# Performance work log

Measured on AMD Instinct MI355X. Metric: run time of the kernel, lower is better.

The kernel has to match this reference:

```python
import jax, jax.numpy as jnp
import numpy as np

B, S, D_MODEL = 1, 1024, 1024
D_CKV, D_CQ = 256, 512
N_HEAD, D_HEAD, D_ROPE = 8, 64, 32


def setup_inputs() -> dict:
    key = jax.random.key(0)
    ks = jax.random.split(key, 12)
    def w(k, shape):
        return jax.random.normal(k, shape, dtype=jnp.float32) * 0.02
    return {
        "x": jax.random.normal(ks[0], (B, S, D_MODEL), dtype=jnp.float32),
        "w_q_idx": w(ks[1], (D_MODEL, N_HEAD * D_HEAD)),
        "w_k_idx": w(ks[2], (D_MODEL, D_HEAD)),
        "w_idx": jnp.ones((N_HEAD,), dtype=jnp.float32),
        "raw_delta": jnp.zeros((D_ROPE // 2,), dtype=jnp.float32),
        "w_dkv": w(ks[3], (D_MODEL, D_CKV)),
        "w_uk": w(ks[4], (D_CKV, N_HEAD * D_HEAD)),
        "w_uv": w(ks[5], (D_CKV, N_HEAD * D_HEAD)),
        "w_dq": w(ks[6], (D_MODEL, D_CQ)),
        "w_uq": w(ks[7], (D_CQ, N_HEAD * D_HEAD)),
        "w_qr": w(ks[8], (D_CQ, N_HEAD * D_ROPE)),
        "w_kr": w(ks[9], (D_MODEL, D_ROPE)),
        "w_out": w(ks[10], (N_HEAD * D_HEAD, D_MODEL)),
        "k_ts": 128,
        "local_window": 64,
    }


def _pope(x, raw_delta, theta):
    # x: (b, L, H, d_rope); positions run along axis 1 (matches torch PoPE)
    delta = -2.0 * jnp.pi * jax.nn.sigmoid(raw_delta)            # (d2,)
    pos = jnp.arange(x.shape[1], dtype=x.dtype)
    ang = pos[None, :, None, None] * theta + delta               # (1, L, 1, d2)
    c, s = jnp.cos(ang), jnp.sin(ang)
    mu1, mu2 = jnp.split(jax.nn.softplus(x), 2, axis=-1)
    return jnp.concatenate((mu1 * c - mu2 * s, mu1 * s + mu2 * c), axis=-1)


def reference(x, w_q_idx, w_k_idx, w_idx, raw_delta, w_dkv, w_uk, w_uv,
              w_dq, w_uq, w_qr, w_kr, w_out, k_ts, local_window):
    b, s, _ = x.shape
    h, dh, dr = N_HEAD, D_HEAD, D_ROPE
    theta = 1.0 / (10000.0 ** (2.0 * jnp.arange(dr // 2, dtype=jnp.float32) / dr))

    # ---- LightningIndexer: per-head relu'd relevance, combined with learned head weights
    qI = (x @ w_q_idx).reshape(b, s, h, dh)
    kI = x @ w_k_idx                                             # (b, s, dh)
    sc = jax.nn.relu(jnp.einsum('bthd,bsd->bths', qI, kI))
    I = jnp.einsum('bths,h->bts', sc, w_idx)

    # ---- TokenSelector: force local window in, mask future out, top-k indices
    qp = jnp.arange(s)[:, None]
    kp = jnp.arange(s)[None, :]
    local = (kp >= qp - local_window + 1) & (kp <= qp)
    causal = kp > qp
    I = jnp.where(local, jnp.inf, I)
    I = jnp.where(causal, -jnp.inf, I)
    k = min(k_ts, s)
    _, idx = jax.lax.top_k(I, k)                                 # (b, s, k) int32

    gather = jax.vmap(lambda t, i: t[i])                         # (s,d),(l,k)->(l,k,d)

    # ---- MLA latent KV, gathered per query
    c_kv = x @ w_dkv                                             # (b, s, d_ckv)
    ckv_sel = gather(c_kv, idx)                                  # (b, s, k, d_ckv)
    key_c = (ckv_sel @ w_uk).reshape(b, s, k, h, dh).transpose(0, 3, 1, 2, 4)
    value = (ckv_sel @ w_uv).reshape(b, s, k, h, dh).transpose(0, 3, 1, 2, 4)

    c_q = x @ w_dq
    query_c = (c_q @ w_uq).reshape(b, s, h, dh).transpose(0, 2, 1, 3)
    query_r = _pope((c_q @ w_qr).reshape(b, s, h, dr), raw_delta, theta).transpose(0, 2, 1, 3)

    # key rope: PoPE applied with positions along the k (selected-token) axis,
    # exactly as the torch code's permute(0,2,1,3) does
    x_sel = gather(x, idx)                                       # (b, s, k, d_model)
    kr = _pope((x_sel @ w_kr).transpose(0, 2, 1, 3), raw_delta, theta).transpose(0, 2, 1, 3)
    key_r = jnp.broadcast_to(kr[:, None], (b, h, s, k, dr))

    query = jnp.concatenate((query_c, query_r), axis=-1)         # (b, h, s, dh+dr)
    keyt = jnp.concatenate((key_c, key_r), axis=-1)              # (b, h, s, k, dh+dr)
    scale = (dh + dr) ** -0.5
    scores = jnp.einsum('bhld,bhlkd->bhlk', query, keyt) * scale
    attn = jax.nn.softmax(scores, axis=-1)
    out = jnp.einsum('bhlk,bhlkd->bhld', attn, value)
    out = out.transpose(0, 2, 1, 3).reshape(b, s, h * dh)
    return out @ w_out
```

## Files before the change

kernel.cpp:

```cpp
#include <hip/hip_runtime.h>
#include <math.h>

#define S_LEN 1024
#define NH 8

typedef __attribute__((ext_vector_type(8))) short bf16x8;
typedef __attribute__((ext_vector_type(4))) float f32x4;

__device__ __forceinline__ float sp_softplus(float x) {
    return fmaxf(x, 0.f) + log1pf(expf(-fabsf(x)));
}

__device__ __forceinline__ unsigned short bfu(float f) {
    unsigned u = __float_as_uint(f);
    unsigned r = (u + 0x7FFFu + ((u >> 16) & 1u)) >> 16;
    return (unsigned short)r;
}

struct FRONT {
    const float *x, *wqidx, *wkidx, *raw_delta, *wuk;
    const float *wdkv, *wdq, *wkr, *wuq, *wqr, *wuv, *wout;
    float *qIP, *kIP, *csc, *css;
    unsigned short *wdkvT, *wdqT, *wkrT, *wuqT, *wqrT, *wuvT, *woutT, *wukb;
};

__global__ __launch_bounds__(256) void front_kernel(FRONT f)
{
    __shared__ float As[2][16][18];
    __shared__ float Bs[2][16][68];
    __shared__ unsigned short tile[64][65];
    int bx = blockIdx.x;
    if (bx < 1152) {
        int gx = bx % 18, gy = bx / 18;
        int half = threadIdx.x >> 7;
        int t = threadIdx.x & 127;
        int u = gx * 2 + half;
        const float* B; float* C;
        int ldb, N, n0, kb;
        if (u < 32) {
            B = f.wqidx; ldb = 512; N = 512;
            C = f.qIP + (long)(u >> 3) * 524288;
            n0 = (u & 7) * 64;
            kb = (u >> 3) * 256;
        } else {
            B = f.wkidx; ldb = 64; N = 64;
            C = f.kIP + (long)(u - 32) * 65536;
            n0 = 0;
            kb = (u - 32) * 256;
        }
        int ke = kb + 256;
        int m0 = gy * 16;
        int ar = t >> 2, ak = t & 3;
        int bk = t >> 3, bn = t & 7;
        int ty = t >> 4, tx = t & 15;

        float4 aN = make_float4(0.f, 0.f, 0.f, 0.f);
        if (t < 64) aN = *(const float4*)(f.x + (long)(m0 + ar) * 1024 + kb + ak * 4);
        float4 b0 = *(const float4*)(B + (long)(kb + bk) * ldb + n0 + bn * 4);
        float4 b1 = *(const float4*)(B + (long)(kb + bk) * ldb + n0 + (bn + 8) * 4);
        float acc[2][4] = {};
        for (int k0 = kb; k0 < ke; k0 += 16) {
            if (t < 64) {
                As[half][ak * 4 + 0][ar] = aN.x;
                As[half][ak * 4 + 1][ar] = aN.y;
                As[half][ak * 4 + 2][ar] = aN.z;
                As[half][ak * 4 + 3][ar] = aN.w;
            }
            *(float4*)&Bs[half][bk][bn * 4] = b0;
            *(float4*)&Bs[half][bk][(bn + 8) * 4] = b1;
            __syncthreads();
            if (k0 + 16 < ke) {
                if (t < 64) aN = *(const float4*)(f.x + (long)(m0 + ar) * 1024 + (k0 + 16) + ak * 4);
                b0 = *(const float4*)(B + (long)(k0 + 16 + bk) * ldb + n0 + bn * 4);
                b1 = *(const float4*)(B + (long)(k0 + 16 + bk) * ldb + n0 + (bn + 8) * 4);
            }
            #pragma unroll
            for (int kk = 0; kk < 16; ++kk) {
                float2 a = *(float2*)&As[half][kk][ty * 2];
                float4 b = *(float4*)&Bs[half][kk][tx * 4];
                acc[0][0] += a.x * b.x; acc[0][1] += a.x * b.y;
                acc[0][2] += a.x * b.z; acc[0][3] += a.x * b.w;
                acc[1][0] += a.y * b.x; acc[1][1] += a.y * b.y;
                acc[1][2] += a.y * b.z; acc[1][3] += a.y * b.w;
            }
            __syncthreads();
        }
        #pragma unroll
        for (int i = 0; i < 2; ++i) {
            float4 v = make_float4(acc[i][0], acc[i][1], acc[i][2], acc[i][3]);
            *(float4*)(C + (long)(m0 + ty * 2 + i) * N + n0 + tx * 4) = v;
        }
    } else if (bx < 1616) {
        int b = bx - 1152;
        const float* srcs[7] = {f.wdkv, f.wdq, f.wkr, f.wuq, f.wqr, f.wuv, f.wout};
        unsigned short* dsts[7] = {f.wdkvT, f.wdqT, f.wkrT, f.wuqT, f.wqrT, f.wuvT, f.woutT};
        const int Ns[7]   = {256, 512, 32, 512, 256, 512, 1024};
        const int Klds[7] = {1024, 1024, 1024, 512, 512, 256, 512};
        const int Ntl[7]  = {4, 8, 1, 8, 4, 8, 16};
        const int bst[8]  = {0, 64, 192, 208, 272, 304, 336, 464};
        int e = 0;
        #pragma unroll
        for (int i = 1; i < 7; ++i) if (b >= bst[i]) e = i;
        int lb = b - bst[e];
        int nt = lb % Ntl[e], kt = lb / Ntl[e];
        const float* src = srcs[e];
        unsigned short* dst = dsts[e];
        int N = Ns[e], Kld = Klds[e];
        int k0 = kt * 64, n0 = nt * 64;
        int t = threadIdx.x;
        int c = t & 63, r4 = t >> 6;
        #pragma unroll
        for (int it = 0; it < 16; ++it) {
            int r = it * 4 + r4;
            float v = (n0 + c < N) ? src[(long)(k0 + r) * N + n0 + c] : 0.f;
            tile[r][c] = bfu(v);
        }
        __syncthreads();
        int wq = t & 7;
        #pragma unroll
        for (int itw = 0; itw < 2; ++itw) {
            int wr = itw * 32 + (t >> 3);
            if (n0 + wr < N) {
                unsigned short v[8];
                #pragma unroll
                for (int j = 0; j < 8; ++j) v[j] = tile[wq * 8 + j][wr];
                *(uint4*)(dst + (long)(n0 + wr) * Kld + k0 + wq * 8) = *(uint4*)v;
            }
        }
    } else if (bx < 1624) {
        int idx = (bx - 1616) * 256 + threadIdx.x;
        int j = idx >> 4, i = idx & 15;
        float rd = f.raw_delta[i];
        float delta = -6.283185307179586f * (1.f / (1.f + expf(-rd)));
        float th = exp2f(-(float)i * 0.83048202372184f);
        float ang = (float)j * th + delta;
        float sv, cv;
        sincosf(ang, &sv, &cv);
        f.csc[idx] = cv;
        f.css[idx] = sv;
    } else {
        int idx = (bx - 1624) * 256 + threadIdx.x;
        f.wukb[idx] = bfu(f.wuk[idx]);
    }
}

__device__ __forceinline__ void mgemm_body(
    const float* A, const unsigned short* B, float* C,
    int lda, int ldb, int ldc, int K, int N, int obf, int m0, int n0, char* smem)
{
    unsigned short (*As)[40] = (unsigned short(*)[40])smem;
    unsigned short (*Bs)[40] = (unsigned short(*)[40])(smem + 5120);
    int t = threadIdx.x;
    int srow = t >> 2, skq = t & 3;
    int wid = t >> 6, l = t & 63;
    int wm = (wid >> 1) * 32, wn = (wid & 1) * 32;
    int fr = l & 15, fk = (l >> 4) * 8;
    bool bok = (n0 + srow) < N;

    f32x4 acc00 = {0.f, 0.f, 0.f, 0.f};
    f32x4 acc01 = {0.f, 0.f, 0.f, 0.f};
    f32x4 acc10 = {0.f, 0.f, 0.f, 0.f};
    f32x4 acc11 = {0.f, 0.f, 0.f, 0.f};

    for (int k0 = 0; k0 < K; k0 += 32) {
        {
            const float* ap = A + (long)(m0 + srow) * lda + k0 + skq * 8;
            float4 v0 = *(const float4*)ap;
            float4 v1 = *(const float4*)(ap + 4);
            unsigned short* d = &As[srow][skq * 8];
            d[0] = bfu(v0.x); d[1] = bfu(v0.y); d[2] = bfu(v0.z); d[3] = bfu(v0.w);
            d[4] = bfu(v1.x); d[5] = bfu(v1.y); d[6] = bfu(v1.z); d[7] = bfu(v1.w);
        }
        {
            uint4 bv = make_uint4(0u, 0u, 0u, 0u);
            if (bok) bv = *(const uint4*)(B + (long)(n0 + srow) * ldb + k0 + skq * 8);
            *(uint4*)&Bs[srow][skq * 8] = bv;
        }
        __syncthreads();
        bf16x8 a0 = *(bf16x8*)&As[wm + fr][fk];
        bf16x8 a1 = *(bf16x8*)&As[wm + 16 + fr][fk];
        bf16x8 b0 = *(bf16x8*)&Bs[wn + fr][fk];
        bf16x8 b1 = *(bf16x8*)&Bs[wn + 16 + fr][fk];
        acc00 = __builtin_amdgcn_mfma_f32_16x16x32_bf16(a0, b0, acc00, 0, 0, 0);
        acc01 = __builtin_amdgcn_mfma_f32_16x16x32_bf16(a0, b1, acc01, 0, 0, 0);
        acc10 = __builtin_amdgcn_mfma_f32_16x16x32_bf16(a1, b0, acc10, 0, 0, 0);
        acc11 = __builtin_amdgcn_mfma_f32_16x16x32_bf16(a1, b1, acc11, 0, 0, 0);
        __syncthreads();
    }
    int crow = (l >> 4) * 4;
    int col0 = n0 + wn + fr, col1 = n0 + wn + 16 + fr;
    if (obf) {
        unsigned short* Cu = (unsigned short*)C;
        if (col0 < N) {
            #pragma unroll
            for (int r = 0; r < 4; ++r) {
                Cu[(long)(m0 + wm + crow + r) * ldc + col0]      = bfu(acc00[r]);
                Cu[(long)(m0 + wm + 16 + crow + r) * ldc + col0] = bfu(acc10[r]);
            }
        }
        if (col1 < N) {
            #pragma unroll
            for (int r = 0; r < 4; ++r) {
                Cu[(long)(m0 + wm + crow + r) * ldc + col1]      = bfu(acc01[r]);
                Cu[(long)(m0 + wm + 16 + crow + r) * ldc + col1] = bfu(acc11[r]);
            }
        }
    } else {
        if (col0 < N) {
            #pragma unroll
            for (int r = 0; r < 4; ++r) {
                C[(long)(m0 + wm + crow + r) * ldc + col0]      = acc00[r];
                C[(long)(m0 + wm + 16 + crow + r) * ldc + col0] = acc10[r];
            }
        }
        if (col1 < N) {
            #pragma unroll
            for (int r = 0; r < 4; ++r) {
                C[(long)(m0 + wm + crow + r) * ldc + col1]      = acc01[r];
                C[(long)(m0 + wm + 16 + crow + r) * ldc + col1] = acc11[r];
            }
        }
    }
}

__device__ __forceinline__ void indexer_body(
    const float* qIP, const float* kIP, const float* w_idx, float* I,
    int b, char* smem)
{
    int sb = b % 16, tb = b / 16;
    if (sb * 64 > tb * 32 + 31) return;
    int t0 = tb * 32, s0 = sb * 64;
    float (*ksT)[68] = (float(*)[68])smem;
    float (*qs)[68]  = (float(*)[68])(smem + 17408);
    int t = threadIdx.x;
    {
        int r = t & 63, q = t >> 6;
        #pragma unroll
        for (int u = 0; u < 4; ++u) {
            int c4 = q * 4 + u;
            long off = (long)(s0 + r) * 64 + c4 * 4;
            float4 v = *(const float4*)(kIP + off);
            #pragma unroll
            for (int s = 1; s < 4; ++s) {
                float4 v2 = *(const float4*)(kIP + (long)s * 65536 + off);
                v.x += v2.x; v.y += v2.y; v.z += v2.z; v.w += v2.w;
            }
            ksT[c4 * 4 + 0][r] = v.x;
            ksT[c4 * 4 + 1][r] = v.y;
            ksT[c4 * 4 + 2][r] = v.z;
            ksT[c4 * 4 + 3][r] = v.w;
        }
    }
    int ty = t >> 4, tx = t & 15;
    float accI[2][4] = {};
    for (int h = 0; h < 8; ++h) {
        __syncthreads();
        {
            int r = t >> 3, q = t & 7;
            long base = (long)(t0 + r) * 512 + h * 64;
            #pragma unroll
            for (int half = 0; half < 2; ++half) {
                long off = base + (q + half * 8) * 4;
                float4 a = *(const float4*)(qIP + off);
                #pragma unroll
                for (int s = 1; s < 4; ++s) {
                    float4 a1 = *(const float4*)(qIP + (long)s * 524288 + off);
                    a.x += a1.x; a.y += a1.y; a.z += a1.z; a.w += a1.w;
                }
                *(float4*)&qs[r][(q + half * 8) * 4] = a;
            }
        }
        __syncthreads();
        float acc[2][4] = {};
        #pragma unroll
        for (int dc = 0; dc < 4; ++dc) {
            float a0[16], a1[16];
            #pragma unroll
            for (int u = 0; u < 4; ++u) {
                float4 v0 = *(float4*)&qs[ty * 2][dc * 16 + u * 4];
                float4 v1 = *(float4*)&qs[ty * 2 + 1][dc * 16 + u * 4];
                a0[u * 4 + 0] = v0.x; a0[u * 4 + 1] = v0.y; a0[u * 4 + 2] = v0.z; a0[u * 4 + 3] = v0.w;
                a1[u * 4 + 0] = v1.x; a1[u * 4 + 1] = v1.y; a1[u * 4 + 2] = v1.z; a1[u * 4 + 3] = v1.w;
            }
            #pragma unroll
            for (int kk = 0; kk < 16; ++kk) {
                int d = dc * 16 + kk;
                float4 bb = *(float4*)&ksT[d][tx * 4];
                acc[0][0] += a0[kk] * bb.x; acc[0][1] += a0[kk] * bb.y;
                acc[0][2] += a0[kk] * bb.z; acc[0][3] += a0[kk] * bb.w;
                acc[1][0] += a1[kk] * bb.x; acc[1][1] += a1[kk] * bb.y;
                acc[1][2] += a1[kk] * bb.z; acc[1][3] += a1[kk] * bb.w;
            }
        }
        float wh = w_idx[h];
        #pragma unroll
        for (int i = 0; i < 2; ++i)
            #pragma unroll
            for (int j = 0; j < 4; ++j)
                accI[i][j] += wh * fmaxf(acc[i][j], 0.f);
    }
    #pragma unroll
    for (int i = 0; i < 2; ++i) {
        float4 v = make_float4(accI[i][0], accI[i][1], accI[i][2], accI[i][3]);
        *(float4*)&I[(long)(t0 + ty * 2 + i) * 1024 + s0 + tx * 4] = v;
    }
}

__device__ __forceinline__ void topk_body(
    const float* I, int* idxout, int b)
{
    int t = b * 4 + (threadIdx.x >> 6);
    int lane = threadIdx.x & 63;
    int smin = max(0, t - 63);
    int w = min(64, t + 1);
    if (lane < w) idxout[t * 128 + lane] = smin + lane;
    for (int q = t + 1 + lane; q < 128; q += 64)
        idxout[t * 128 + q] = q;
    int f = max(0, t - 63);
    int m = min(f, 64);
    if (m == 0) return;
    const float* row = I + (long)t * 1024;

    unsigned long long key[16];
    #pragma unroll
    for (int g4 = 0; g4 < 4; ++g4) {
        float4 v = *(const float4*)(row + lane * 16 + g4 * 4);
        float vv[4] = {v.x, v.y, v.z, v.w};
        #pragma unroll
        for (int j = 0; j < 4; ++j) {
            int s = lane * 16 + g4 * 4 + j;
            unsigned long long k = 0ull;
            if (s < f) {
                unsigned u = __float_as_uint(vv[j]);
                unsigned ou = (u & 0x80000000u) ? ~u : (u | 0x80000000u);
                k = ((unsigned long long)ou << 32) | (0xFFFFFFFFu - (unsigned)s);
            }
            key[g4 * 4 + j] = k;
        }
    }

    #pragma unroll
    for (int km = 1; km <= 10; ++km) {
        #pragma unroll
        for (int jm = km - 1; jm >= 0; --jm) {
            if (jm >= 4) {
                int lmask = 1 << (jm - 4);
                #pragma unroll
                for (int r = 0; r < 16; ++r) {
                    unsigned long long other = __shfl_xor(key[r], lmask, 64);
                    int i = lane * 16 + r;
                    bool keep_max = (((i & (1 << km)) == 0) == ((i & (1 << jm)) == 0));
                    unsigned long long mx = key[r] > other ? key[r] : other;
                    unsigned long long mn = key[r] > other ? other : key[r];
                    key[r] = keep_max ? mx : mn;
                }
            } else {
                int rmask = 1 << jm;
                #pragma unroll
                for (int r = 0; r < 16; ++r) {
                    if ((r & rmask) == 0) {
                        int r2 = r | rmask;
                        int i = lane * 16 + r;
                        bool keep_max_low = ((i & (1 << km)) == 0);
                        unsigned long long a = key[r], b2 = key[r2];
                        unsigned long long mx = a > b2 ? a : b2;
                        unsigned long long mn = a > b2 ? b2 : a;
                        key[r]  = keep_max_low ? mx : mn;
                        key[r2] = keep_max_low ? mn : mx;
                    }
                }
            }
        }
    }

    if (lane < 4) {
        #pragma unroll
        for (int r = 0; r < 16; ++r) {
            int e = lane * 16 + r;
            if (e < m) {
                int s = (int)(0xFFFFFFFFu - (unsigned)(key[r] & 0xFFFFFFFFull));
                idxout[t * 128 + w + e] = s;
            }
        }
    }
}

struct S1ARG {
    const float* x;
    const unsigned short *wdkvT, *wdqT, *wkrT;
    unsigned short* ckvb; float *cq, *xkr;
    const float *qIP, *kIP, *w_idx; float* I;
};

__global__ __launch_bounds__(256) void s1_kernel(S1ARG g)
{
    __shared__ __align__(16) char smem[26112];
    int bx = blockIdx.x;
    if (bx < 208) {
        int xi = bx % 13, m0 = (bx / 13) * 64;
        if (xi < 4)       mgemm_body(g.x, g.wdkvT, (float*)g.ckvb, 1024, 1024, 256, 1024, 256, 1, m0, xi * 64, smem);
        else if (xi < 12) mgemm_body(g.x, g.wdqT,  g.cq,           1024, 1024, 512, 1024, 512, 0, m0, (xi - 4) * 64, smem);
        else              mgemm_body(g.x, g.wkrT,  g.xkr,          1024, 1024, 32,  1024, 32,  0, m0, 0, smem);
    } else {
        indexer_body(g.qIP, g.kIP, g.w_idx, g.I, bx - 208, smem);
    }
}

struct S2ARG {
    const float* cq;
    const unsigned short *wuqT, *wqrT;
    float *qc, *qrp;
    const float* I; int* idxb;
};

__global__ __launch_bounds__(256) void s2_kernel(S2ARG g)
{
    __shared__ __align__(16) char smem[10240];
    int bx = blockIdx.x;
    if (bx < 192) {
        int xi = bx % 12, m0 = (bx / 12) * 64;
        if (xi < 8) mgemm_body(g.cq, g.wuqT, g.qc,  512, 512, 512, 512, 512, 0, m0, xi * 64, smem);
        else        mgemm_body(g.cq, g.wqrT, g.qrp, 512, 512, 256, 512, 256, 0, m0, (xi - 8) * 64, smem);
    } else {
        topk_body(g.I, g.idxb, bx - 192);
    }
}

struct MID2 {
    const float* qc; const unsigned short* wukb; float* qabs;
    const float *qrp, *raw_delta; float* qrr;
    const float* xkr; float* mu;
};

__global__ __launch_bounds__(256) void mid2_kernel(MID2 g)
{
    __shared__ __align__(16) char smem[10240];
    int b = blockIdx.x;
    int t = threadIdx.x;
    if (b < 512) {
        int h = b >> 6, rem = b & 63;
        int n0 = (rem >> 4) * 64, m0 = (rem & 15) * 64;
        mgemm_body(g.qc + h * 64, g.wukb + h * 64, g.qabs + h * 256,
                   512, 512, 2048, 64, 256, 0, m0, n0, smem);
    } else if (b < 1024) {
        int tq = (b - 512) * 2 + (t >> 7);
        int tt = t & 127;
        int h = tt >> 4, i = tt & 15;
        float rd = g.raw_delta[i];
        float delta = -6.283185307179586f * (1.f / (1.f + expf(-rd)));
        float th = exp2f(-(float)i * 0.83048202372184f);
        float ang = (float)tq * th + delta;
        float sv, cv;
        sincosf(ang, &sv, &cv);
        float m1 = sp_softplus(g.qrp[tq * 256 + h * 32 + i]);
        float m2 = sp_softplus(g.qrp[tq * 256 + h * 32 + 16 + i]);
        g.qrr[tq * 256 + h * 32 + i]      = m1 * cv - m2 * sv;
        g.qrr[tq * 256 + h * 32 + 16 + i] = m1 * sv + m2 * cv;
    } else {
        int i = (b - 1024) * 256 + t;
        g.mu[i] = sp_softplus(g.xkr[i]);
    }
}

struct MFG {
    const float* A[10]; const unsigned short* B[10]; float* C[10];
    int lda[10], ldb[10], ldc[10], K[10], N[10], obf[10];
    int tstart[11]; int ne;
};

__global__ __launch_bounds__(256) void mgemm(MFG mg)
{
    __shared__ __align__(16) char smem[10240];
    int bx = blockIdx.x, e = 0;
    #pragma unroll
    for (int i = 1; i < 10; ++i) if (i < mg.ne && bx >= mg.tstart[i]) e = i;
    mgemm_body(mg.A[e], mg.B[e], mg.C[e], mg.lda[e], mg.ldb[e], mg.ldc[e],
               mg.K[e], mg.N[e], mg.obf[e], blockIdx.y * 64,
               (bx - mg.tstart[e]) * 64, smem);
}

__global__ __launch_bounds__(256) void attn_kernel(
    const float* __restrict__ qabs, const float* __restrict__ qrr,
    const unsigned short* __restrict__ ckvb, const float* __restrict__ mu,
    const float* __restrict__ csc, const float* __restrict__ css,
    const int* __restrict__ idxb, float* __restrict__ olat)
{
    __shared__ float sc[8][68];
    __shared__ float hs[16];
    __shared__ int idx_s[128];

    int t = blockIdx.x, tid = threadIdx.x;
    int w = tid >> 6, l = tid & 63;
    const float scale = 0.10206207261596575f;

    if (tid < 128) idx_s[tid] = idxb[t * 128 + tid];

    int hrow = l & 15;
    int kslice = (l >> 4) * 8;
    int hpv = l >> 3;
    int c8 = w * 64 + (l & 7) * 8;

    float mrun0 = -INFINITY, mrun1 = -INFINITY;
    float lrun0 = 0.f, lrun1 = 0.f;
    float acc0 = 0, acc1 = 0, acc2 = 0, acc3 = 0;
    float acc4 = 0, acc5 = 0, acc6 = 0, acc7 = 0;

    __syncthreads();

    #pragma unroll
    for (int chunk = 0; chunk < 2; ++chunk) {
        if (chunk) __syncthreads();

        int r = w * 16 + hrow;
        int src = idx_s[chunk * 64 + r];
        int jglob = chunk * 64 + r;
        f32x4 st = {0.f, 0.f, 0.f, 0.f};
        #pragma unroll 1
        for (int ks = 0; ks < 8; ++ks) {
            bf16x8 af = *(const bf16x8*)(ckvb + (long)src * 256 + ks * 32 + kslice);
            bf16x8 qf = {0, 0, 0, 0, 0, 0, 0, 0};
            if (hrow < 8) {
                const float* qp = qabs + (long)t * 2048 + hrow * 256 + ks * 32 + kslice;
                float4 a = *(const float4*)qp;
                float4 b = *(const float4*)(qp + 4);
                unsigned short qq[8];
                qq[0] = bfu(a.x * scale); qq[1] = bfu(a.y * scale);
                qq[2] = bfu(a.z * scale); qq[3] = bfu(a.w * scale);
                qq[4] = bfu(b.x * scale); qq[5] = bfu(b.y * scale);
                qq[6] = bfu(b.z * scale); qq[7] = bfu(b.w * scale);
                qf = *(bf16x8*)qq;
            }
            st = __builtin_amdgcn_mfma_f32_16x16x32_bf16(af, qf, st, 0, 0, 0);
        }
        {
            int i15 = kslice & 15;
            bool lo = kslice < 16;
            float4 m1a = *(const float4*)(mu + src * 32 + i15);
            float4 m1b = *(const float4*)(mu + src * 32 + i15 + 4);
            float4 m2a = *(const float4*)(mu + src * 32 + 16 + i15);
            float4 m2b = *(const float4*)(mu + src * 32 + 16 + i15 + 4);
            float4 ca = *(const float4*)(csc + jglob * 16 + i15);
            float4 cb = *(const float4*)(csc + jglob * 16 + i15 + 4);
            float4 sa = *(const float4*)(css + jglob * 16 + i15);
            float4 sb = *(const float4*)(css + jglob * 16 + i15 + 4);
            unsigned short hh[8];
            hh[0] = bfu(lo ? m1a.x * ca.x - m2a.x * sa.x : m1a.x * sa.x + m2a.x * ca.x);
            hh[1] = bfu(lo ? m1a.y * ca.y - m2a.y * sa.y : m1a.y * sa.y + m2a.y * ca.y);
            hh[2] = bfu(lo ? m1a.z * ca.z - m2a.z * sa.z : m1a.z * sa.z + m2a.z * ca.z);
            hh[3] = bfu(lo ? m1a.w * ca.w - m2a.w * sa.w : m1a.w * sa.w + m2a.w * ca.w);
            hh[4] = bfu(lo ? m1b.x * cb.x - m2b.x * sb.x : m1b.x * sb.x + m2b.x * cb.x);
            hh[5] = bfu(lo ? m1b.y * cb.y - m2b.y * sb.y : m1b.y * sb.y + m2b.y * cb.y);
            hh[6] = bfu(lo ? m1b.z * cb.z - m2b.z * sb.z : m1b.z * sb.z + m2b.z * cb.z);
            hh[7] = bfu(lo ? m1b.w * cb.w - m2b.w * sb.w : m1b.w * sb.w + m2b.w * cb.w);
            bf16x8 af = *(bf16x8*)hh;
            bf16x8 qf = {0, 0, 0, 0, 0, 0, 0, 0};
            if (hrow < 8) {
                const float* qp = qrr + (long)t * 256 + hrow * 32 + kslice;
                float4 a = *(const float4*)qp;
                float4 b = *(const float4*)(qp + 4);
                unsigned short qq[8];
                qq[0] = bfu(a.x * scale); qq[1] = bfu(a.y * scale);
                qq[2] = bfu(a.z * scale); qq[3] = bfu(a.w * scale);
                qq[4] = bfu(b.x * scale); qq[5] = bfu(b.y * scale);
                qq[6] = bfu(b.z * scale); qq[7] = bfu(b.w * scale);
                qf = *(bf16x8*)qq;
            }
            st = __builtin_amdgcn_mfma_f32_16x16x32_bf16(af, qf, st, 0, 0, 0);
        }
        {
            int srow2 = w * 16 + (l >> 4) * 4;
            if (hrow < 8) {
                #pragma unroll
                for (int rr = 0; rr < 4; ++rr) sc[hrow][srow2 + rr] = st[rr];
            }
        }
        __syncthreads();

        float rh0, rh1;
        {
            int h = 2 * w;
            float v = sc[h][l];
            float mx = v;
            #pragma unroll
            for (int off = 32; off > 0; off >>= 1) mx = fmaxf(mx, __shfl_xor(mx, off));
            float mnew = fmaxf(mrun0, mx);
            float p = expf(v - mnew);
            float ps = p;
            #pragma unroll
            for (int off = 32; off > 0; off >>= 1) ps += __shfl_xor(ps, off);
            rh0 = expf(mrun0 - mnew);
            lrun0 = lrun0 * rh0 + ps;
            mrun0 = mnew;
            sc[h][l] = p;
        }
        {
            int h = 2 * w + 1;
            float v = sc[h][l];
            float mx = v;
            #pragma unroll
            for (int off = 32; off > 0; off >>= 1) mx = fmaxf(mx, __shfl_xor(mx, off));
            float mnew = fmaxf(mrun1, mx);
            float p = expf(v - mnew);
            float ps = p;
            #pragma unroll
            for (int off = 32; off > 0; off >>= 1) ps += __shfl_xor(ps, off);
            rh1 = expf(mrun1 - mnew);
            lrun1 = lrun1 * rh1 + ps;
            mrun1 = mnew;
            sc[h][l] = p;
        }
        if (l == 0) {
            hs[2 * w] = rh0;
            hs[2 * w + 1] = rh1;
            if (chunk == 1) {
                hs[8 + 2 * w] = lrun0;
                hs[8 + 2 * w + 1] = lrun1;
            }
        }
        __syncthreads();

        float rsel = hs[hpv];
        acc0 *= rsel; acc1 *= rsel; acc2 *= rsel; acc3 *= rsel;
        acc4 *= rsel; acc5 *= rsel; acc6 *= rsel; acc7 *= rsel;
        #pragma unroll 4
        for (int j = 0; j < 64; ++j) {
            float p = sc[hpv][j];
            int srcj = idx_s[chunk * 64 + j];
            uint4 vv = *(const uint4*)(ckvb + (long)srcj * 256 + c8);
            acc0 += p * __uint_as_float(vv.x << 16);
            acc1 += p * __uint_as_float(vv.x & 0xffff0000u);
            acc2 += p * __uint_as_float(vv.y << 16);
            acc3 += p * __uint_as_float(vv.y & 0xffff0000u);
            acc4 += p * __uint_as_float(vv.z << 16);
            acc5 += p * __uint_as_float(vv.z & 0xffff0000u);
            acc6 += p * __uint_as_float(vv.w << 16);
            acc7 += p * __uint_as_float(vv.w & 0xffff0000u);
        }
    }

    float inv = 1.f / hs[8 + hpv];
    float* op = olat + (long)t * 2048 + hpv * 256 + c8;
    *(float4*)op       = make_float4(acc0 * inv, acc1 * inv, acc2 * inv, acc3 * inv);
    *(float4*)(op + 4) = make_float4(acc4 * inv, acc5 * inv, acc6 * inv, acc7 * inv);
}

extern "C" void kernel_launch(void* const* d_in, const int* in_sizes, int n_in,
                              void* d_out, int out_size, void* d_ws, size_t ws_size,
                              hipStream_t stream)
{
    const float* x         = (const float*)d_in[0];
    const float* w_q_idx   = (const float*)d_in[1];
    const float* w_k_idx   = (const float*)d_in[2];
    const float* w_idx     = (const float*)d_in[3];
    const float* raw_delta = (const float*)d_in[4];
    const float* w_dkv     = (const float*)d_in[5];
    const float* w_uk      = (const float*)d_in[6];
    const float* w_uv      = (const float*)d_in[7];
    const float* w_dq      = (const float*)d_in[8];
    const float* w_uq      = (const float*)d_in[9];
    const float* w_qr      = (const float*)d_in[10];
    const float* w_kr      = (const float*)d_in[11];
    const float* w_out     = (const float*)d_in[12];
    (void)in_sizes; (void)n_in; (void)out_size; (void)ws_size;
    float* out = (float*)d_out;

    float* ws = (float*)d_ws;
    unsigned short* ckvb = (unsigned short*)ws;   ws += 131072;
    float* cq    = ws;        ws += 1024 * 512;
    float* xkr   = ws;        ws += 1024 * 32;
    float* qrp   = ws;        ws += 1024 * 256;
    float* qrr   = ws;        ws += 1024 * 256;
    float* qc    = ws;        ws += 1024 * 512;
    float* qabs  = ws;        ws += 1024 * 2048;
    float* Ibuf  = ws;        ws += 1024 * 1024;
    int*   idxb  = (int*)ws;  ws += 1024 * 128;
    float* olat  = ws;        ws += 1024 * 2048;
    float* outh  = ws;        ws += 1024 * 512;
    float* mu    = ws;        ws += 1024 * 32;
    float* cscb  = ws;        ws += 128 * 16;
    float* cssb  = ws;        ws += 128 * 16;
    unsigned short* wdkvT = (unsigned short*)ws;  ws += 131072;
    unsigned short* wdqT  = (unsigned short*)ws;  ws += 262144;
    unsigned short* wkrT  = (unsigned short*)ws;  ws += 16384;
    unsigned short* wuqT  = (unsigned short*)ws;  ws += 131072;
    unsigned short* wqrT  = (unsigned short*)ws;  ws += 65536;
    unsigned short* wuvT  = (unsigned short*)ws;  ws += 65536;
    unsigned short* woutT = (unsigned short*)ws;  ws += 262144;
    unsigned short* wukb  = (unsigned short*)ws;  ws += 65536;
    float* part  = ws;        ws += 2359296;
    float* qIP = part;
    float* kIP = part + 2097152;

    {
        FRONT f{};
        f.x = x; f.wqidx = w_q_idx; f.wkidx = w_k_idx; f.raw_delta = raw_delta; f.wuk = w_uk;
        f.wdkv = w_dkv; f.wdq = w_dq; f.wkr = w_kr; f.wuq = w_uq; f.wqr = w_qr;
        f.wuv = w_uv; f.wout = w_out;
        f.qIP = qIP; f.kIP = kIP; f.csc = cscb; f.css = cssb;
        f.wdkvT = wdkvT; f.wdqT = wdqT; f.wkrT = wkrT; f.wuqT = wuqT;
        f.wqrT = wqrT; f.wuvT = wuvT; f.woutT = woutT; f.wukb = wukb;
        front_kernel<<<dim3(2136), dim3(256), 0, stream>>>(f);
    }

    {
        S1ARG g{};
        g.x = x; g.wdkvT = wdkvT; g.wdqT = wdqT; g.wkrT = wkrT;
        g.ckvb = ckvb; g.cq = cq; g.xkr = xkr;
        g.qIP = qIP; g.kIP = kIP; g.w_idx = w_idx; g.I = Ibuf;
        s1_kernel<<<dim3(720), dim3(256), 0, stream>>>(g);
    }

    {
        S2ARG g{};
        g.cq = cq; g.wuqT = wuqT; g.wqrT = wqrT;
        g.qc = qc; g.qrp = qrp;
        g.I = Ibuf; g.idxb = idxb;
        s2_kernel<<<dim3(448), dim3(256), 0, stream>>>(g);
    }

    {
        MID2 g{};
        g.qc = qc; g.wukb = wukb; g.qabs = qabs;
        g.qrp = qrp; g.raw_delta = raw_delta; g.qrr = qrr;
        g.xkr = xkr; g.mu = mu;
        mid2_kernel<<<dim3(1152), dim3(256), 0, stream>>>(g);
    }

    attn_kernel<<<dim3(1024), dim3(256), 0, stream>>>(qabs, qrr, ckvb, mu, cscb, cssb, idxb, olat);

    {
        MFG m{};
        for (int h = 0; h < 8; ++h) {
            m.A[h] = olat + h * 256;      m.lda[h] = 2048; m.K[h] = 256;
            m.B[h] = wuvT + h * 64 * 256; m.ldb[h] = 256;
            m.C[h] = outh + h * 64;       m.ldc[h] = 512;  m.N[h] = 64;
            m.tstart[h] = h;
        }
        m.tstart[8] = 8;
        m.ne = 8;
        mgemm<<<dim3(8, 16), dim3(256), 0, stream>>>(m);
    }

    {
        MFG m{};
        m.A[0] = outh;  m.lda[0] = 512; m.K[0] = 512;
        m.B[0] = woutT; m.ldb[0] = 512;
        m.C[0] = out;   m.ldc[0] = 1024; m.N[0] = 1024;
        m.tstart[0] = 0; m.tstart[1] = 16;
        m.ne = 1;
        mgemm<<<dim3(16, 16), dim3(256), 0, stream>>>(m);
    }
}
```

Measured before the change: 163.8 us.

## Rebalance kernel stages to co-schedule independent work across launches

Work is redistributed across the launch sequence. The indexer partial GEMMs move out of the front kernel into a new kernel alongside the x-projection GEMMs. The indexer scoring runs alongside the cq up-projections, and top-k runs alongside the q absorption and rope work. Independent tasks now share grids, aiming to balance per-kernel work and reduce idle tail time between dependent stages, at the cost of a different dependency ordering and more heterogeneous blocks per launch.

```diff
diff --git a/kernel.cpp b/kernel.cpp
--- a/kernel.cpp
+++ b/kernel.cpp
@@ -17,81 +17,19 @@
     return (unsigned short)r;
 }
 
-struct FRONT {
-    const float *x, *wqidx, *wkidx, *raw_delta, *wuk;
+struct PREP {
+    const float *raw_delta, *wuk;
     const float *wdkv, *wdq, *wkr, *wuq, *wqr, *wuv, *wout;
-    float *qIP, *kIP, *csc, *css;
+    float *csc, *css;
     unsigned short *wdkvT, *wdqT, *wkrT, *wuqT, *wqrT, *wuvT, *woutT, *wukb;
 };
 
-__global__ __launch_bounds__(256) void front_kernel(FRONT f)
-{
-    __shared__ float As[2][16][18];
-    __shared__ float Bs[2][16][68];
+__global__ __launch_bounds__(256) void prep_kernel(PREP f)
+{
     __shared__ unsigned short tile[64][65];
     int bx = blockIdx.x;
-    if (bx < 1152) {
-        int gx = bx % 18, gy = bx / 18;
-        int half = threadIdx.x >> 7;
-        int t = threadIdx.x & 127;
-        int u = gx * 2 + half;
-        const float* B; float* C;
-        int ldb, N, n0, kb;
-        if (u < 32) {
-            B = f.wqidx; ldb = 512; N = 512;
-            C = f.qIP + (long)(u >> 3) * 524288;
-            n0 = (u & 7) * 64;
-            kb = (u >> 3) * 256;
-        } else {
-            B = f.wkidx; ldb = 64; N = 64;
-            C = f.kIP + (long)(u - 32) * 65536;
-            n0 = 0;
-            kb = (u - 32) * 256;
-        }
-        int ke = kb + 256;
-        int m0 = gy * 16;
-        int ar = t >> 2, ak = t & 3;
-        int bk = t >> 3, bn = t & 7;
-        int ty = t >> 4, tx = t & 15;
-
-        float4 aN = make_float4(0.f, 0.f, 0.f, 0.f);
-        if (t < 64) aN = *(const float4*)(f.x + (long)(m0 + ar) * 1024 + kb + ak * 4);
-        float4 b0 = *(const float4*)(B + (long)(kb + bk) * ldb + n0 + bn * 4);
-        float4 b1 = *(const float4*)(B + (long)(kb + bk) * ldb + n0 + (bn + 8) * 4);
-        float acc[2][4] = {};
-        for (int k0 = kb; k0 < ke; k0 += 16) {
-            if (t < 64) {
-                As[half][ak * 4 + 0][ar] = aN.x;
-                As[half][ak * 4 + 1][ar] = aN.y;
-                As[half][ak * 4 + 2][ar] = aN.z;
-                As[half][ak * 4 + 3][ar] = aN.w;
-            }
-            *(float4*)&Bs[half][bk][bn * 4] = b0;
-            *(float4*)&Bs[half][bk][(bn + 8) * 4] = b1;
-            __syncthreads();
-            if (k0 + 16 < ke) {
-                if (t < 64) aN = *(const float4*)(f.x + (long)(m0 + ar) * 1024 + (k0 + 16) + ak * 4);
-                b0 = *(const float4*)(B + (long)(k0 + 16 + bk) * ldb + n0 + bn * 4);
-                b1 = *(const float4*)(B + (long)(k0 + 16 + bk) * ldb + n0 + (bn + 8) * 4);
-            }
-            #pragma unroll
-            for (int kk = 0; kk < 16; ++kk) {
-                float2 a = *(float2*)&As[half][kk][ty * 2];
-                float4 b = *(float4*)&Bs[half][kk][tx * 4];
-                acc[0][0] += a.x * b.x; acc[0][1] += a.x * b.y;
-                acc[0][2] += a.x * b.z; acc[0][3] += a.x * b.w;
-                acc[1][0] += a.y * b.x; acc[1][1] += a.y * b.y;
-                acc[1][2] += a.y * b.z; acc[1][3] += a.y * b.w;
-            }
-            __syncthreads();
-        }
-        #pragma unroll
-        for (int i = 0; i < 2; ++i) {
-            float4 v = make_float4(acc[i][0], acc[i][1], acc[i][2], acc[i][3]);
-            *(float4*)(C + (long)(m0 + ty * 2 + i) * N + n0 + tx * 4) = v;
-        }
-    } else if (bx < 1616) {
-        int b = bx - 1152;
+    if (bx < 464) {
+        int b = bx;
         const float* srcs[7] = {f.wdkv, f.wdq, f.wkr, f.wuq, f.wqr, f.wuv, f.wout};
         unsigned short* dsts[7] = {f.wdkvT, f.wdqT, f.wkrT, f.wuqT, f.wqrT, f.wuvT, f.woutT};
         const int Ns[7]   = {256, 512, 32, 512, 256, 512, 1024};
@@ -127,8 +65,8 @@
                 *(uint4*)(dst + (long)(n0 + wr) * Kld + k0 + wq * 8) = *(uint4*)v;
             }
         }
-    } else if (bx < 1624) {
-        int idx = (bx - 1616) * 256 + threadIdx.x;
+    } else if (bx < 472) {
+        int idx = (bx - 464) * 256 + threadIdx.x;
         int j = idx >> 4, i = idx & 15;
         float rd = f.raw_delta[i];
         float delta = -6.283185307179586f * (1.f / (1.f + expf(-rd)));
@@ -139,7 +77,7 @@
         f.csc[idx] = cv;
         f.css[idx] = sv;
     } else {
-        int idx = (bx - 1624) * 256 + threadIdx.x;
+        int idx = (bx - 472) * 256 + threadIdx.x;
         f.wukb[idx] = bfu(f.wuk[idx]);
     }
 }
@@ -220,6 +158,88 @@
                 C[(long)(m0 + wm + 16 + crow + r) * ldc + col1] = acc11[r];
             }
         }
+    }
+}
+
+struct SELV {
+    const float *x, *wqidx, *wkidx;
+    const unsigned short *wdkvT, *wdqT, *wkrT;
+    unsigned short* ckvb; float *cq, *xkr;
+    float *qIP, *kIP;
+};
+
+__global__ __launch_bounds__(256) void selv_kernel(SELV g)
+{
+    __shared__ __align__(16) char smem[11008];
+    int bx = blockIdx.x;
+    if (bx < 208) {
+        int xi = bx % 13, m0 = (bx / 13) * 64;
+        if (xi < 4)       mgemm_body(g.x, g.wdkvT, (float*)g.ckvb, 1024, 1024, 256, 1024, 256, 1, m0, xi * 64, smem);
+        else if (xi < 12) mgemm_body(g.x, g.wdqT,  g.cq,           1024, 1024, 512, 1024, 512, 0, m0, (xi - 4) * 64, smem);
+        else              mgemm_body(g.x, g.wkrT,  g.xkr,          1024, 1024, 32,  1024, 32,  0, m0, 0, smem);
+        return;
+    }
+    float (*As)[16][18] = (float(*)[16][18])smem;
+    float (*Bs)[16][68] = (float(*)[16][68])(smem + 2304);
+    int b = bx - 208;
+    int gx = b % 18, gy = b / 18;
+    int half = threadIdx.x >> 7;
+    int t = threadIdx.x & 127;
+    int u = gx * 2 + half;
+    const float* B; float* C;
+    int ldb, N, n0, kb;
+    if (u < 32) {
+        B = g.wqidx; ldb = 512; N = 512;
+        C = g.qIP + (long)(u >> 3) * 524288;
+        n0 = (u & 7) * 64;
+        kb = (u >> 3) * 256;
+    } else {
+        B = g.wkidx; ldb = 64; N = 64;
+        C = g.kIP + (long)(u - 32) * 65536;
+        n0 = 0;
+        kb = (u - 32) * 256;
+    }
+    int ke = kb + 256;
+    int m0 = gy * 16;
+    int ar = t >> 2, ak = t & 3;
+    int bk = t >> 3, bn = t & 7;
+    int ty = t >> 4, tx = t & 15;
+
+    float4 aN = make_float4(0.f, 0.f, 0.f, 0.f);
+    if (t < 64) aN = *(const float4*)(g.x + (long)(m0 + ar) * 1024 + kb + ak * 4);
+    float4 b0 = *(const float4*)(B + (long)(kb + bk) * ldb + n0 + bn * 4);
+    float4 b1 = *(const float4*)(B + (long)(kb + bk) * ldb + n0 + (bn + 8) * 4);
+    float acc[2][4] = {};
+    for (int k0 = kb; k0 < ke; k0 += 16) {
+        if (t < 64) {
+            As[half][ak * 4 + 0][ar] = aN.x;
+            As[half][ak * 4 + 1][ar] = aN.y;
+            As[half][ak * 4 + 2][ar] = aN.z;
+            As[half][ak * 4 + 3][ar] = aN.w;
+        }
+        *(float4*)&Bs[half][bk][bn * 4] = b0;
+        *(float4*)&Bs[half][bk][(bn + 8) * 4] = b1;
+        __syncthreads();
+        if (k0 + 16 < ke) {
+            if (t < 64) aN = *(const float4*)(g.x + (long)(m0 + ar) * 1024 + (k0 + 16) + ak * 4);
+            b0 = *(const float4*)(B + (long)(k0 + 16 + bk) * ldb + n0 + bn * 4);
+            b1 = *(const float4*)(B + (long)(k0 + 16 + bk) * ldb + n0 + (bn + 8) * 4);
+        }
+        #pragma unroll
+        for (int kk = 0; kk < 16; ++kk) {
+            float2 a = *(float2*)&As[half][kk][ty * 2];
+            float4 bb = *(float4*)&Bs[half][kk][tx * 4];
+            acc[0][0] += a.x * bb.x; acc[0][1] += a.x * bb.y;
+            acc[0][2] += a.x * bb.z; acc[0][3] += a.x * bb.w;
+            acc[1][0] += a.y * bb.x; acc[1][1] += a.y * bb.y;
+            acc[1][2] += a.y * bb.z; acc[1][3] += a.y * bb.w;
+        }
+        __syncthreads();
+    }
+    #pragma unroll
+    for (int i = 0; i < 2; ++i) {
+        float4 v = make_float4(acc[i][0], acc[i][1], acc[i][2], acc[i][3]);
+        *(float4*)(C + (long)(m0 + ty * 2 + i) * N + n0 + tx * 4) = v;
     }
 }
 
@@ -385,65 +405,48 @@
     }
 }
 
-struct S1ARG {
-    const float* x;
-    const unsigned short *wdkvT, *wdqT, *wkrT;
-    unsigned short* ckvb; float *cq, *xkr;
-    const float *qIP, *kIP, *w_idx; float* I;
-};
-
-__global__ __launch_bounds__(256) void s1_kernel(S1ARG g)
-{
-    __shared__ __align__(16) char smem[26112];
-    int bx = blockIdx.x;
-    if (bx < 208) {
-        int xi = bx % 13, m0 = (bx / 13) * 64;
-        if (xi < 4)       mgemm_body(g.x, g.wdkvT, (float*)g.ckvb, 1024, 1024, 256, 1024, 256, 1, m0, xi * 64, smem);
-        else if (xi < 12) mgemm_body(g.x, g.wdqT,  g.cq,           1024, 1024, 512, 1024, 512, 0, m0, (xi - 4) * 64, smem);
-        else              mgemm_body(g.x, g.wkrT,  g.xkr,          1024, 1024, 32,  1024, 32,  0, m0, 0, smem);
-    } else {
-        indexer_body(g.qIP, g.kIP, g.w_idx, g.I, bx - 208, smem);
-    }
-}
-
-struct S2ARG {
+struct S2C {
     const float* cq;
     const unsigned short *wuqT, *wqrT;
     float *qc, *qrp;
-    const float* I; int* idxb;
+    const float *qIP, *kIP, *w_idx; float* I;
 };
 
-__global__ __launch_bounds__(256) void s2_kernel(S2ARG g)
-{
-    __shared__ __align__(16) char smem[10240];
+__global__ __launch_bounds__(256) void s2c_kernel(S2C g)
+{
+    __shared__ __align__(16) char smem[26112];
     int bx = blockIdx.x;
     if (bx < 192) {
         int xi = bx % 12, m0 = (bx / 12) * 64;
         if (xi < 8) mgemm_body(g.cq, g.wuqT, g.qc,  512, 512, 512, 512, 512, 0, m0, xi * 64, smem);
         else        mgemm_body(g.cq, g.wqrT, g.qrp, 512, 512, 256, 512, 256, 0, m0, (xi - 8) * 64, smem);
     } else {
-        topk_body(g.I, g.idxb, bx - 192);
-    }
-}
-
-struct MID2 {
+        indexer_body(g.qIP, g.kIP, g.w_idx, g.I, bx - 192, smem);
+    }
+}
+
+struct MID3 {
+    const float* I; int* idxb;
     const float* qc; const unsigned short* wukb; float* qabs;
     const float *qrp, *raw_delta; float* qrr;
     const float* xkr; float* mu;
 };
 
-__global__ __launch_bounds__(256) void mid2_kernel(MID2 g)
+__global__ __launch_bounds__(256) void mid3_kernel(MID3 g)
 {
     __shared__ __align__(16) char smem[10240];
     int b = blockIdx.x;
     int t = threadIdx.x;
-    if (b < 512) {
-        int h = b >> 6, rem = b & 63;
+    if (b < 256) {
+        topk_body(g.I, g.idxb, b);
+    } else if (b < 768) {
+        int lb = b - 256;
+        int h = lb >> 6, rem = lb & 63;
         int n0 = (rem >> 4) * 64, m0 = (rem & 15) * 64;
         mgemm_body(g.qc + h * 64, g.wukb + h * 64, g.qabs + h * 256,
                    512, 512, 2048, 64, 256, 0, m0, n0, smem);
-    } else if (b < 1024) {
-        int tq = (b - 512) * 2 + (t >> 7);
+    } else if (b < 1280) {
+        int tq = (b - 768) * 2 + (t >> 7);
         int tt = t & 127;
         int h = tt >> 4, i = tt & 15;
         float rd = g.raw_delta[i];
@@ -457,7 +460,7 @@
         g.qrr[tq * 256 + h * 32 + i]      = m1 * cv - m2 * sv;
         g.qrr[tq * 256 + h * 32 + 16 + i] = m1 * sv + m2 * cv;
     } else {
-        int i = (b - 1024) * 256 + t;
+        int i = (b - 1280) * 256 + t;
         g.mu[i] = sp_softplus(g.xkr[i]);
     }
 }
@@ -692,38 +695,40 @@
     float* kIP = part + 2097152;
 
     {
-        FRONT f{};
-        f.x = x; f.wqidx = w_q_idx; f.wkidx = w_k_idx; f.raw_delta = raw_delta; f.wuk = w_uk;
+        PREP f{};
+        f.raw_delta = raw_delta; f.wuk = w_uk;
         f.wdkv = w_dkv; f.wdq = w_dq; f.wkr = w_kr; f.wuq = w_uq; f.wqr = w_qr;
         f.wuv = w_uv; f.wout = w_out;
-        f.qIP = qIP; f.kIP = kIP; f.csc = cscb; f.css = cssb;
+        f.csc = cscb; f.css = cssb;
         f.wdkvT = wdkvT; f.wdqT = wdqT; f.wkrT = wkrT; f.wuqT = wuqT;
         f.wqrT = wqrT; f.wuvT = wuvT; f.woutT = woutT; f.wukb = wukb;
-        front_kernel<<<dim3(2136), dim3(256), 0, stream>>>(f);
+        prep_kernel<<<dim3(984), dim3(256), 0, stream>>>(f);
     }
 
     {
-        S1ARG g{};
-        g.x = x; g.wdkvT = wdkvT; g.wdqT = wdqT; g.wkrT = wkrT;
+        SELV g{};
+        g.x = x; g.wqidx = w_q_idx; g.wkidx = w_k_idx;
+        g.wdkvT = wdkvT; g.wdqT = wdqT; g.wkrT = wkrT;
         g.ckvb = ckvb; g.cq = cq; g.xkr = xkr;
-        g.qIP = qIP; g.kIP = kIP; g.w_idx = w_idx; g.I = Ibuf;
-        s1_kernel<<<dim3(720), dim3(256), 0, stream>>>(g);
+        g.qIP = qIP; g.kIP = kIP;
+        selv_kernel<<<dim3(1360), dim3(256), 0, stream>>>(g);
     }
 
     {
-        S2ARG g{};
+        S2C g{};
         g.cq = cq; g.wuqT = wuqT; g.wqrT = wqrT;
         g.qc = qc; g.qrp = qrp;
+        g.qIP = qIP; g.kIP = kIP; g.w_idx = w_idx; g.I = Ibuf;
+        s2c_kernel<<<dim3(704), dim3(256), 0, stream>>>(g);
+    }
+
+    {
+        MID3 g{};
         g.I = Ibuf; g.idxb = idxb;
-        s2_kernel<<<dim3(448), dim3(256), 0, stream>>>(g);
-    }
-
-    {
-        MID2 g{};
         g.qc = qc; g.wukb = wukb; g.qabs = qabs;
         g.qrp = qrp; g.raw_delta = raw_delta; g.qrr = qrr;
         g.xkr = xkr; g.mu = mu;
-        mid2_kernel<<<dim3(1152), dim3(256), 0, stream>>>(g);
+        mid3_kernel<<<dim3(1408), dim3(256), 0, stream>>>(g);
     }
 
     attn_kernel<<<dim3(1024), dim3(256), 0, stream>>>(qabs, qrr, ckvb, mu, cscb, cssb, idxb, olat);
```

Result: slower. 170.9 us (+4.4%).
